# Kernel tuning notes

Measured on AMD Instinct MI355X. Metric: run time of the kernel, lower is better.

The kernel has to match this reference:

```python
import jax, jax.numpy as jnp
import numpy as np

B, IN, OUT = 8192, 4096, 4096
EPS = 1e-4


def setup_inputs() -> dict:
    key = jax.random.key(0)
    k1, k2 = jax.random.split(key)
    x = jax.random.normal(k1, (B, IN), dtype=jnp.float32)
    gamma = jnp.ones((IN,), dtype=jnp.float32)
    beta = jnp.zeros((IN,), dtype=jnp.float32)
    weight = jax.random.normal(k2, (OUT, IN), dtype=jnp.float32) * 0.02
    bias = jnp.zeros((OUT,), dtype=jnp.float32)
    return {"x": x, "gamma": gamma, "beta": beta, "weight": weight, "bias": bias}


def bin_weight(w):
    # center per output row, clamp, L1-scale, sign (2D branch of BinWeightFn)
    wc = jnp.clip(w - jnp.mean(w, axis=1, keepdims=True), -1.0, 1.0)
    n = w.shape[1]
    scale = jnp.sum(jnp.abs(wc), axis=1, keepdims=True) / n  # [out, 1]
    return jnp.sign(wc), scale


def reference(x, gamma, beta, weight, bias):
    # BatchNorm1d in training mode: batch statistics (biased variance)
    mu = jnp.mean(x, axis=0)
    var = jnp.var(x, axis=0)
    xn = (x - mu) / jnp.sqrt(var + EPS) * gamma + beta
    # binarize activations and weights
    x_bin = jnp.sign(xn)
    w_bin, scale = bin_weight(weight)
    # binary GEMM + bias, then per-output-channel L1 scale, then ReLU
    y = x_bin @ w_bin.T + bias          # [B, OUT]
    y = y * scale.reshape(1, -1)
    return jax.nn.relu(y)
```

## Files before the change

### kernel.cpp

```cpp
#include <hip/hip_runtime.h>
#include <stdint.h>

#define BATCH 8192
#define IN 4096
#define OUT 4096
#define EPS 1e-4f
#define RCHUNK 128
#define NCHUNKS (BATCH / RCHUNK)

typedef int v4i __attribute__((ext_vector_type(4)));
typedef unsigned char u8;

#define AS1(p) ((const __attribute__((address_space(1))) void*)(p))
#define AS3(p) ((__attribute__((address_space(3))) void*)(p))

__global__ __launch_bounds__(256) void colstat_partial(
    const float* __restrict__ x, float* __restrict__ P1, float* __restrict__ P2) {
    int c4 = blockIdx.x * 256 + threadIdx.x;
    int r0 = blockIdx.y * RCHUNK;
    float4 s1 = {0.f, 0.f, 0.f, 0.f}, s2 = {0.f, 0.f, 0.f, 0.f};
    const float4* p = (const float4*)x + (size_t)r0 * (IN / 4) + c4;
#pragma unroll 8
    for (int r = 0; r < RCHUNK; ++r) {
        float4 v = p[(size_t)r * (IN / 4)];
        s1.x += v.x; s1.y += v.y; s1.z += v.z; s1.w += v.w;
        s2.x += v.x * v.x; s2.y += v.y * v.y; s2.z += v.z * v.z; s2.w += v.w * v.w;
    }
    ((float4*)P1)[blockIdx.y * (IN / 4) + c4] = s1;
    ((float4*)P2)[blockIdx.y * (IN / 4) + c4] = s2;
}

__global__ __launch_bounds__(256) void colstat_final(
    const float* __restrict__ P1, const float* __restrict__ P2,
    const float* __restrict__ gamma, float* __restrict__ mu, float* __restrict__ aArr) {
    int col = blockIdx.x * 256 + threadIdx.x;
    double s1 = 0.0, s2 = 0.0;
#pragma unroll 4
    for (int c = 0; c < NCHUNKS; ++c) {
        s1 += (double)P1[c * IN + col];
        s2 += (double)P2[c * IN + col];
    }
    double m = s1 / (double)BATCH;
    double var = s2 / (double)BATCH - m * m;
    float rstd = (float)(1.0 / sqrt(var + (double)EPS));
    mu[col] = (float)m;
    aArr[col] = rstd * gamma[col];
}

__global__ __launch_bounds__(256) void binxw(
    const float* __restrict__ x, const float* __restrict__ mu,
    const float* __restrict__ aArr, const float* __restrict__ beta,
    const float* __restrict__ w,
    u8* __restrict__ x01, int* __restrict__ px,
    u8* __restrict__ w01, float* __restrict__ scale, int* __restrict__ pw) {
    __shared__ double redd[4];
    __shared__ int redi[4];
    __shared__ double bcast;
    int tid = threadIdx.x;
    int lane = tid & 63;
    int wv = tid >> 6;

    if (blockIdx.x < OUT) {
        int o = blockIdx.x;
        const float4* row = (const float4*)(w + (size_t)o * IN);
        uchar4* o4 = (uchar4*)(w01 + (size_t)o * IN);

        float4 vs[4];
        float part = 0.f;
#pragma unroll
        for (int it = 0; it < 4; ++it) {
            vs[it] = row[it * 256 + tid];
            part += vs[it].x + vs[it].y + vs[it].z + vs[it].w;
        }
        double d = (double)part;
        for (int off = 32; off > 0; off >>= 1) d += __shfl_down(d, off, 64);
        if (lane == 0) redd[wv] = d;
        __syncthreads();
        if (tid == 0) bcast = (redd[0] + redd[1] + redd[2] + redd[3]) / (double)IN;
        __syncthreads();
        float mean = (float)bcast;

        float absacc = 0.f;
        int cnt = 0;
#pragma unroll
        for (int it = 0; it < 4; ++it) {
            float4 v = vs[it];
            float wcx = v.x - mean, wcy = v.y - mean, wcz = v.z - mean, wcw = v.w - mean;
            uchar4 ob;
            ob.x = (u8)(wcx > 0.f);
            ob.y = (u8)(wcy > 0.f);
            ob.z = (u8)(wcz > 0.f);
            ob.w = (u8)(wcw > 0.f);
            cnt += (int)ob.x + (int)ob.y + (int)ob.z + (int)ob.w;
            absacc += fminf(fabsf(wcx), 1.0f) + fminf(fabsf(wcy), 1.0f) +
                      fminf(fabsf(wcz), 1.0f) + fminf(fabsf(wcw), 1.0f);
            o4[it * 256 + tid] = ob;
        }
        double da = (double)absacc;
        for (int off = 32; off > 0; off >>= 1) da += __shfl_down(da, off, 64);
        for (int off = 32; off > 0; off >>= 1) cnt += __shfl_down(cnt, off, 64);
        if (lane == 0) { redd[wv] = da; redi[wv] = cnt; }
        __syncthreads();
        if (tid == 0) {
            scale[o] = (float)((redd[0] + redd[1] + redd[2] + redd[3]) / (double)IN);
            pw[o] = redi[0] + redi[1] + redi[2] + redi[3];
        }
    } else {
        int r = blockIdx.x - OUT;
        const float4* row = (const float4*)(x + (size_t)r * IN);
        const float4* m4 = (const float4*)mu;
        const float4* a4 = (const float4*)aArr;
        const float4* b4 = (const float4*)beta;
        uchar4* o4 = (uchar4*)(x01 + (size_t)r * IN);
        int cnt = 0;
#pragma unroll
        for (int it = 0; it < IN / 1024; ++it) {
            int q = it * 256 + tid;
            float4 v = row[q];
            float4 m = m4[q];
            float4 a = a4[q];
            float4 b = b4[q];
            uchar4 ob;
            ob.x = (u8)((v.x - m.x) * a.x + b.x > 0.f);
            ob.y = (u8)((v.y - m.y) * a.y + b.y > 0.f);
            ob.z = (u8)((v.z - m.z) * a.z + b.z > 0.f);
            ob.w = (u8)((v.w - m.w) * a.w + b.w > 0.f);
            cnt += (int)ob.x + (int)ob.y + (int)ob.z + (int)ob.w;
            o4[q] = ob;
        }
        for (int off = 32; off > 0; off >>= 1) cnt += __shfl_down(cnt, off, 64);
        if (lane == 0) redi[wv] = cnt;
        __syncthreads();
        if (tid == 0) px[r] = redi[0] + redi[1] + redi[2] + redi[3];
    }
}

#define BK2 64
#define NT2 (IN / BK2)

#define STG2_A(t, q) __builtin_amdgcn_global_load_lds( \
    AS1(ag + (size_t)((q)*128 + slr2) * IN + (t)*BK2 + sswz2), \
    AS3(lds + ((t)&3)*32768 + (q)*8192 + sdst2), 16, 0, 0)
#define STG2_B(t, q) __builtin_amdgcn_global_load_lds( \
    AS1(bg + (size_t)((q)*128 + slr2) * IN + (t)*BK2 + sswz2), \
    AS3(lds + ((t)&3)*32768 + 16384 + (q)*8192 + sdst2), 16, 0, 0)
#define STG2(t) do { STG2_A(t,0); STG2_A(t,1); STG2_B(t,0); STG2_B(t,1); } while (0)

#define RD(t) do { \
    const u8* bp_ = lds + ((t)&3)*32768; \
    _Pragma("unroll") for (int j_ = 0; j_ < 4; ++j_) \
        bf[j_] = *(const v4i*)(bp_ + bB + j_*1024); \
    _Pragma("unroll") for (int i_ = 0; i_ < 8; ++i_) \
        af[i_] = *(const v4i*)(bp_ + aB + i_*1024); \
} while (0)

#define MMA2() do { \
    __builtin_amdgcn_s_setprio(1); \
    _Pragma("unroll") for (int i_ = 0; i_ < 8; ++i_) \
    _Pragma("unroll") for (int j_ = 0; j_ < 4; ++j_) \
        acc[i_][j_] = __builtin_amdgcn_mfma_i32_16x16x64_i8( \
            af[i_], bf[j_], acc[i_][j_], 0, 0, 0); \
    __builtin_amdgcn_s_setprio(0); \
} while (0)

#define BAR() asm volatile("s_barrier" ::: "memory")
#define VM(n) asm volatile("s_waitcnt vmcnt(" #n ")" ::: "memory")

__global__ __launch_bounds__(512, 2) void bgemm_i8(
    const u8* __restrict__ x01, const u8* __restrict__ w01,
    const int* __restrict__ px, const int* __restrict__ pw,
    const float* __restrict__ scale, const float* __restrict__ bias,
    float* __restrict__ out) {
    __shared__ u8 lds[131072];

    int tid = threadIdx.x;
    int lane = tid & 63;
    int wave = tid >> 6;
    int wm = wave >> 2;
    int wn = wave & 3;

    int lin = blockIdx.y * (OUT / 256) + blockIdx.x;
    int swz = (lin & 7) * 64 + (lin >> 3);
    int colBlk = (swz & 15) * 256;
    int rowBlk = (swz >> 4) * 256;

    const u8* ag = x01 + (size_t)rowBlk * IN;
    const u8* bg = w01 + (size_t)colBlk * IN;

    int slr2 = tid >> 2;
    int ss2 = tid & 3;
    int sxor = (slr2 & 3) ^ ((slr2 >> 2) & 3);
    int sswz2 = (ss2 ^ sxor) * 16;
    int sdst2 = slr2 * 64 + ss2 * 16;

    int lrow = lane & 15;
    int lhi = lane >> 4;
    int rxor = (lrow & 3) ^ ((lrow >> 2) & 3);
    int swk2 = (lhi ^ rxor) * 16;
    int aB = (wm * 128 + lrow) * 64 + swk2;
    int bB = 16384 + (wn * 64 + lrow) * 64 + swk2;

    v4i acc[8][4];
#pragma unroll
    for (int i = 0; i < 8; ++i)
#pragma unroll
        for (int j = 0; j < 4; ++j) acc[i][j] = (v4i){0, 0, 0, 0};
    v4i af[8], bf[4];

    STG2(0); STG2(1); STG2(2);
    VM(8);
    BAR();

    for (int tt = 0; tt < 15; ++tt) {
        int t0 = tt * 4;
#pragma unroll
        for (int u = 0; u < 4; ++u) {
            int t = t0 + u;
            RD(t);
            STG2(t + 3);
            MMA2();
            VM(8);
            BAR();
        }
    }
    RD(60); STG2(63); MMA2(); VM(8); BAR();
    RD(61); MMA2(); VM(4); BAR();
    RD(62); MMA2(); VM(0); BAR();
    RD(63); MMA2();

    int crow0 = lhi * 4;
    int ccol = lrow;
#pragma unroll
    for (int i = 0; i < 8; ++i) {
        int rbase = rowBlk + wm * 128 + i * 16 + crow0;
        int pxr[4];
#pragma unroll
        for (int rg = 0; rg < 4; ++rg) pxr[rg] = px[rbase + rg];
#pragma unroll
        for (int j = 0; j < 4; ++j) {
            int cb = colBlk + wn * 64 + j * 16 + ccol;
            float sc = scale[cb];
            float bs = bias[cb];
            int pwc = pw[cb];
#pragma unroll
            for (int rg = 0; rg < 4; ++rg) {
                int dot = 4 * acc[i][j][rg] - 2 * pxr[rg] - 2 * pwc + IN;
                float y = ((float)dot + bs) * sc;
                out[(size_t)(rbase + rg) * OUT + cb] = y > 0.f ? y : 0.f;
            }
        }
    }
}

extern "C" void kernel_launch(void* const* d_in, const int* in_sizes, int n_in,
                              void* d_out, int out_size, void* d_ws, size_t ws_size,
                              hipStream_t stream) {
    const float* x = (const float*)d_in[0];
    const float* gamma = (const float*)d_in[1];
    const float* beta = (const float*)d_in[2];
    const float* weight = (const float*)d_in[3];
    const float* bias = (const float*)d_in[4];
    float* out = (float*)d_out;

    char* w = (char*)d_ws;
    float* mu = (float*)(w);
    float* aArr = (float*)(w + 16384);
    float* scale = (float*)(w + 32768);
    int* px = (int*)(w + 49152);
    int* pw = (int*)(w + 81920);
    float* P1 = (float*)(w + (1 << 20));
    float* P2 = (float*)(w + (2 << 20));
    u8* x01 = (u8*)(w + (4 << 20));
    u8* w01 = (u8*)(w + (36 << 20));

    colstat_partial<<<dim3(IN / 1024, NCHUNKS), 256, 0, stream>>>(x, P1, P2);
    colstat_final<<<dim3(IN / 256), 256, 0, stream>>>(P1, P2, gamma, mu, aArr);
    binxw<<<dim3(OUT + BATCH), 256, 0, stream>>>(x, mu, aArr, beta, weight,
                                                 x01, px, w01, scale, pw);
    bgemm_i8<<<dim3(OUT / 256, BATCH / 256), 512, 0, stream>>>(x01, w01, px, pw, scale, bias, out);
}
```

Before: 409.4 us.

## Double the K tile to 128 and switch to a double-buffered LDS pipeline

The binary int8 GEMM now stages 128-wide K tiles into two 64KB LDS buffers instead of 64-wide tiles in a four-slot ring. This halves the number of barrier and wait steps per output tile. LDS fragment loads are now interleaved with the MFMA issue per A-row, and the XOR swizzle is widened to 8 chunks to match 128-byte rows. The trade-off is a prefetch distance of one tile with full vmcnt(0) waits, which may expose global-load latency that the deeper ring used to hide.

```diff
diff --git a/kernel.cpp b/kernel.cpp
--- a/kernel.cpp
+++ b/kernel.cpp
@@ -135,32 +135,38 @@
     }
 }
 
-#define BK2 64
-#define NT2 (IN / BK2)
-
-#define STG2_A(t, q) __builtin_amdgcn_global_load_lds( \
-    AS1(ag + (size_t)((q)*128 + slr2) * IN + (t)*BK2 + sswz2), \
-    AS3(lds + ((t)&3)*32768 + (q)*8192 + sdst2), 16, 0, 0)
-#define STG2_B(t, q) __builtin_amdgcn_global_load_lds( \
-    AS1(bg + (size_t)((q)*128 + slr2) * IN + (t)*BK2 + sswz2), \
-    AS3(lds + ((t)&3)*32768 + 16384 + (q)*8192 + sdst2), 16, 0, 0)
-#define STG2(t) do { STG2_A(t,0); STG2_A(t,1); STG2_B(t,0); STG2_B(t,1); } while (0)
-
-#define RD(t) do { \
-    const u8* bp_ = lds + ((t)&3)*32768; \
+#define BKB 128
+#define NKT (IN / BKB)
+
+#define STG_A(t, q, p) __builtin_amdgcn_global_load_lds( \
+    AS1(ag + (size_t)((q)*64 + slr) * IN + (t)*BKB + sswz), \
+    AS3(lds + (p)*65536 + (q)*8192 + sdst), 16, 0, 0)
+#define STG_B(t, q, p) __builtin_amdgcn_global_load_lds( \
+    AS1(bg + (size_t)((q)*64 + slr) * IN + (t)*BKB + sswz), \
+    AS3(lds + (p)*65536 + 32768 + (q)*8192 + sdst), 16, 0, 0)
+#define STG8(t, p) do { \
+    STG_A(t, 0, p); STG_A(t, 1, p); STG_A(t, 2, p); STG_A(t, 3, p); \
+    STG_B(t, 0, p); STG_B(t, 1, p); STG_B(t, 2, p); STG_B(t, 3, p); \
+} while (0)
+
+#define RD_MMA(p) do { \
+    const u8* bp_ = lds + (p)*65536; \
+    v4i bfr[4][2]; \
     _Pragma("unroll") for (int j_ = 0; j_ < 4; ++j_) \
-        bf[j_] = *(const v4i*)(bp_ + bB + j_*1024); \
-    _Pragma("unroll") for (int i_ = 0; i_ < 8; ++i_) \
-        af[i_] = *(const v4i*)(bp_ + aB + i_*1024); \
-} while (0)
-
-#define MMA2() do { \
-    __builtin_amdgcn_s_setprio(1); \
-    _Pragma("unroll") for (int i_ = 0; i_ < 8; ++i_) \
-    _Pragma("unroll") for (int j_ = 0; j_ < 4; ++j_) \
-        acc[i_][j_] = __builtin_amdgcn_mfma_i32_16x16x64_i8( \
-            af[i_], bf[j_], acc[i_][j_], 0, 0, 0); \
-    __builtin_amdgcn_s_setprio(0); \
+    _Pragma("unroll") for (int k_ = 0; k_ < 2; ++k_) \
+        bfr[j_][k_] = *(const v4i*)(bp_ + bBase + j_*2048 + swk[k_]); \
+    _Pragma("unroll") for (int i_ = 0; i_ < 8; ++i_) { \
+        v4i a0_ = *(const v4i*)(bp_ + aBase + i_*2048 + swk[0]); \
+        v4i a1_ = *(const v4i*)(bp_ + aBase + i_*2048 + swk[1]); \
+        __builtin_amdgcn_s_setprio(1); \
+        _Pragma("unroll") for (int j_ = 0; j_ < 4; ++j_) { \
+            acc[i_][j_] = __builtin_amdgcn_mfma_i32_16x16x64_i8( \
+                a0_, bfr[j_][0], acc[i_][j_], 0, 0, 0); \
+            acc[i_][j_] = __builtin_amdgcn_mfma_i32_16x16x64_i8( \
+                a1_, bfr[j_][1], acc[i_][j_], 0, 0, 0); \
+        } \
+        __builtin_amdgcn_s_setprio(0); \
+    } \
 } while (0)
 
 #define BAR() asm volatile("s_barrier" ::: "memory")
@@ -187,46 +193,41 @@
     const u8* ag = x01 + (size_t)rowBlk * IN;
     const u8* bg = w01 + (size_t)colBlk * IN;
 
-    int slr2 = tid >> 2;
-    int ss2 = tid & 3;
-    int sxor = (slr2 & 3) ^ ((slr2 >> 2) & 3);
-    int sswz2 = (ss2 ^ sxor) * 16;
-    int sdst2 = slr2 * 64 + ss2 * 16;
+    int slr = tid >> 3;
+    int ss = tid & 7;
+    int sswz = (ss ^ (slr & 7)) * 16;
+    int sdst = slr * 128 + ss * 16;
 
     int lrow = lane & 15;
     int lhi = lane >> 4;
-    int rxor = (lrow & 3) ^ ((lrow >> 2) & 3);
-    int swk2 = (lhi ^ rxor) * 16;
-    int aB = (wm * 128 + lrow) * 64 + swk2;
-    int bB = 16384 + (wn * 64 + lrow) * 64 + swk2;
+    int llo = lane & 7;
+    int swk[2] = { ((lhi) ^ llo) * 16, ((4 + lhi) ^ llo) * 16 };
+    int aBase = (wm * 128 + lrow) * 128;
+    int bBase = 32768 + (wn * 64 + lrow) * 128;
 
     v4i acc[8][4];
 #pragma unroll
     for (int i = 0; i < 8; ++i)
 #pragma unroll
         for (int j = 0; j < 4; ++j) acc[i][j] = (v4i){0, 0, 0, 0};
-    v4i af[8], bf[4];
-
-    STG2(0); STG2(1); STG2(2);
-    VM(8);
+
+    STG8(0, 0);
+    VM(0);
     BAR();
 
     for (int tt = 0; tt < 15; ++tt) {
-        int t0 = tt * 4;
-#pragma unroll
-        for (int u = 0; u < 4; ++u) {
-            int t = t0 + u;
-            RD(t);
-            STG2(t + 3);
-            MMA2();
-            VM(8);
-            BAR();
-        }
-    }
-    RD(60); STG2(63); MMA2(); VM(8); BAR();
-    RD(61); MMA2(); VM(4); BAR();
-    RD(62); MMA2(); VM(0); BAR();
-    RD(63); MMA2();
+        int t = 2 * tt;
+        STG8(t + 1, 1);
+        RD_MMA(0);
+        VM(0); BAR();
+        STG8(t + 2, 0);
+        RD_MMA(1);
+        VM(0); BAR();
+    }
+    STG8(31, 1);
+    RD_MMA(0);
+    VM(0); BAR();
+    RD_MMA(1);
 
     int crow0 = lhi * 4;
     int ccol = lrow;
```

After: 403.6 us. No clear change (-1.4%).
